# Optimization experiments

Measured on AMD Instinct MI355X. Metric: run time of the kernel, lower is better.

## Reference

```python
import jax, jax.numpy as jnp
import numpy as np

T, D_IN, H, E = 8192, 2048, 2048, 512


def setup_inputs() -> dict:
    key = jax.random.key(0)
    k_x, k_wi, k_wh, k_wo = jax.random.split(key, 4)
    s_in = 1.0 / np.sqrt(D_IN)
    s_h = 1.0 / np.sqrt(H)
    return {
        "inputs": jax.random.normal(k_x, (T, D_IN), dtype=jnp.float32),
        "w_i": jax.random.normal(k_wi, (D_IN, 3 * H), dtype=jnp.float32) * s_in,
        "w_h": jax.random.normal(k_wh, (H, 3 * H), dtype=jnp.float32) * s_h,
        "b": jnp.zeros((3 * H,), dtype=jnp.float32),
        "w_out": jax.random.normal(k_wo, (H, E), dtype=jnp.float32) * s_h,
        "b_out": jnp.zeros((E,), dtype=jnp.float32),
    }


def reference(inputs, w_i, w_h, b, w_out, b_out):
    h_size = w_h.shape[0]
    w_h_zr = w_h[:, : 2 * h_size]   # [H, 2H]
    w_h_a = w_h[:, 2 * h_size :]    # [H, H]
    b_zr = b[: 2 * h_size]
    b_a = b[2 * h_size :]

    def step(h, x):
        gates_x = x @ w_i                       # [3H]
        zr_x = gates_x[: 2 * h_size]
        a_x = gates_x[2 * h_size :]
        zr = jax.nn.sigmoid(zr_x + h @ w_h_zr + b_zr)
        z, r = zr[:h_size], zr[h_size:]
        a = jnp.tanh(a_x + (r * h) @ w_h_a + b_a)
        h_new = (1.0 - z) * h + z * a
        return h_new, None

    h0 = jnp.zeros((h_size,), dtype=inputs.dtype)
    h_final, _ = jax.lax.scan(step, h0, inputs)
    return h_final @ w_out + b_out
```

## Files before the change

### kernel.cpp

```cpp
#include <hip/hip_runtime.h>
#include <stdint.h>

#define T_STEPS 8192
#define DIN     2048
#define HD      2048
#define G3      6144
#define EOUT    512

#define NA 64
#define NB 64
#define HP 1024
#define NREP 8
#define SPIN_MAX (1<<20)

typedef unsigned long long u64;
typedef __attribute__((ext_vector_type(8))) __bf16 bf16x8;
typedef __attribute__((ext_vector_type(8))) unsigned short u16x8;
typedef __attribute__((ext_vector_type(4))) float f32x4;

__device__ __forceinline__ uint16_t f2bf(float v){
  uint32_t x = __float_as_uint(v);
  return (uint16_t)((x + 0x7fffu + ((x >> 16) & 1u)) >> 16);
}

__device__ __forceinline__ u64 aload(const u64* p){
  return __hip_atomic_load(p, __ATOMIC_RELAXED, __HIP_MEMORY_SCOPE_AGENT);
}
__device__ __forceinline__ void astore(u64* p, u64 v){
  __hip_atomic_store(p, v, __ATOMIC_RELAXED, __HIP_MEMORY_SCOPE_AGENT);
}

__device__ __forceinline__ void poll2(const u64* p0, const u64* p1, uint32_t want,
                                      u64& r0, u64& r1, volatile int* deadp){
  u64 a0 = aload(p0), a1 = aload(p1);
  int spins = 0;
  for(;;){
    u64 b0 = aload(p0), b1 = aload(p1);
    if ((uint32_t)(a0 >> 32) >= want && (uint32_t)(a1 >> 32) >= want) break;
    if ((++spins & 63) == 0){
      if (*deadp) break;
      if (spins > SPIN_MAX){ *deadp = 1; break; }
    }
    a0 = b0; a1 = b1;
  }
  r0 = a0; r1 = a1;
}

__device__ __forceinline__ bf16x8 load_afrag(const float* __restrict__ w, int col, int kb){
  u16x8 r;
  #pragma unroll
  for (int j = 0; j < 8; ++j)
    r[j] = f2bf(w[(size_t)(kb + j)*G3 + col]);
  return __builtin_bit_cast(bf16x8, r);
}

__device__ __forceinline__ void mv_pass(const uint32_t* vp_base,
                                        const bf16x8* wA, const bf16x8* wB,
                                        float* red, int wid, int lane){
  const uint32_t* vp = vp_base + wid*128;
  const int boff = (lane >> 4) << 2;
  f32x4 acc0 = {0.f,0.f,0.f,0.f}, acc1 = {0.f,0.f,0.f,0.f};
  #pragma unroll
  for (int s = 0; s < 8; ++s){
    uint4 bu = *(const uint4*)(vp + s*16 + boff);
    bf16x8 bf = __builtin_bit_cast(bf16x8, bu);
    acc0 = __builtin_amdgcn_mfma_f32_16x16x32_bf16(wA[s], bf, acc0, 0, 0, 0);
    acc1 = __builtin_amdgcn_mfma_f32_16x16x32_bf16(wB[s], bf, acc1, 0, 0, 0);
  }
  if ((lane & 15) == 0){
    int mb = (lane >> 4) << 2;
    #pragma unroll
    for (int r = 0; r < 4; ++r){
      red[(mb + r)*9 + wid]      = acc0[r];
      red[(16 + mb + r)*9 + wid] = acc1[r];
    }
  }
}

__global__ __launch_bounds__(512) void gates_gemm(const float* __restrict__ A,
                                                  const float* __restrict__ B,
                                                  float* __restrict__ C){
  __shared__ uint16_t Asb[128*40];
  __shared__ uint16_t Bsb[128*40];
  const int bm = blockIdx.x / (G3/128);
  const int bn = blockIdx.x % (G3/128);
  const int row0 = bm*128, col0 = bn*128;
  const int tid  = threadIdx.x;
  const int lane = tid & 63, wid = tid >> 6;
  const int wr = wid >> 2, wc = wid & 3;
  f32x4 acc[4][2] = {};
  for (int k0 = 0; k0 < DIN; k0 += 32){
    {
      int m = tid >> 2, ks = (tid & 3) * 8;
      const float* src = A + (size_t)(row0 + m)*DIN + k0 + ks;
      float4 f0 = *(const float4*)src;
      float4 f1 = *(const float4*)(src + 4);
      u16x8 pk;
      pk[0]=f2bf(f0.x); pk[1]=f2bf(f0.y); pk[2]=f2bf(f0.z); pk[3]=f2bf(f0.w);
      pk[4]=f2bf(f1.x); pk[5]=f2bf(f1.y); pk[6]=f2bf(f1.z); pk[7]=f2bf(f1.w);
      *(u16x8*)(Asb + m*40 + ks) = pk;
    }
    {
      int k = tid >> 4, n8 = tid & 15;
      const float* src = B + (size_t)(k0 + k)*G3 + col0 + n8;
      #pragma unroll
      for (int i = 0; i < 8; ++i)
        Bsb[(n8 + 16*i)*40 + k] = f2bf(src[16*i]);
    }
    __syncthreads();
    const int mrow = wr*64, ncol = wc*32;
    const int fm = lane & 15, fk = (lane >> 4) * 8;
    bf16x8 bfr[2];
    #pragma unroll
    for (int j = 0; j < 2; ++j)
      bfr[j] = *(const bf16x8*)(Bsb + (ncol + j*16 + fm)*40 + fk);
    #pragma unroll
    for (int i = 0; i < 4; ++i){
      bf16x8 af = *(const bf16x8*)(Asb + (mrow + i*16 + fm)*40 + fk);
      acc[i][0] = __builtin_amdgcn_mfma_f32_16x16x32_bf16(af, bfr[0], acc[i][0], 0,0,0);
      acc[i][1] = __builtin_amdgcn_mfma_f32_16x16x32_bf16(af, bfr[1], acc[i][1], 0,0,0);
    }
    __syncthreads();
  }
  const int mrow = row0 + wr*64, ncol = col0 + wc*32;
  #pragma unroll
  for (int i = 0; i < 4; ++i)
    #pragma unroll
    for (int j = 0; j < 2; ++j){
      int cc = ncol + j*16 + (lane & 15);
      int rr = mrow + i*16 + (lane >> 4)*4;
      #pragma unroll
      for (int q = 0; q < 4; ++q)
        C[(size_t)(rr + q)*G3 + cc] = acc[i][j][q];
    }
}

__global__ __launch_bounds__(512) void scan_kernel(
    const float* __restrict__ gates, const float* __restrict__ w_h,
    const float* __restrict__ b,
    u64* hbuf, u64* rhbuf, float* hfinal)
{
  __shared__ uint32_t vph[2][1024];
  __shared__ uint32_t vprh[2][1024];
  __shared__ float    red0[32*9];
  __shared__ float    red1[32*9];
  __shared__ float    gx[2][64];
  __shared__ float    hloc[2][32];
  __shared__ int      dead;
  volatile int* deadp = &dead;

  const int tid  = threadIdx.x;
  const int lane = tid & 63;
  const int wid  = tid >> 6;
  const bool isA = blockIdx.x < NA;
  const int  g   = isA ? (int)blockIdx.x : (int)blockIdx.x - NA;
  const int  rep = blockIdx.x & (NREP - 1);

  bf16x8 w0[8], w1[8], w2[8], w3[8];
  {
    const int kb0 = wid*256 + ((lane >> 4) << 3);
    const int c0  = isA ? (2048 + 32*g) : (32*g);
    #pragma unroll
    for (int s = 0; s < 8; ++s){
      w0[s] = load_afrag(w_h, c0 + (lane & 15),      kb0 + s*32);
      w1[s] = load_afrag(w_h, c0 + 16 + (lane & 15), kb0 + s*32);
    }
    if (!isA){
      const int ca = 4096 + 32*g;
      #pragma unroll
      for (int s = 0; s < 8; ++s){
        w2[s] = load_afrag(w_h, ca + (lane & 15),      kb0 + s*32);
        w3[s] = load_afrag(w_h, ca + 16 + (lane & 15), kb0 + s*32);
      }
    }
  }

  if (tid == 0) *deadp = 0;
  if (tid < 64) ((float*)hloc)[tid] = 0.f;

  int   gcol = -1;
  float bias = 0.f;
  if (isA) { if (tid < 32) gcol = 2048 + 32*g + tid; }
  else     { if (tid < 32)      gcol = 32*g + tid;
             else if (tid < 64) gcol = 4096 + 32*g + (tid - 32);}
  if (gcol >= 0) { bias = b[gcol]; gx[0][tid] = gates[gcol] + bias; }
  __syncthreads();

  for (int t = 0; t < T_STEPS; ++t){
    const int par = t & 1;

    {
      const u64* src = hbuf + ((size_t)(rep*2 + par))*HP;
      u64 v0, v1;
      poll2(src + tid, src + tid + 512, (uint32_t)t, v0, v1, deadp);
      vph[par][tid]       = (uint32_t)v0;
      vph[par][tid + 512] = (uint32_t)v1;
    }
    __syncthreads();
    if (*deadp) break;

    if (isA){
      mv_pass(&vph[par][0], w0, w1, red0, wid, lane);
      __syncthreads();
      if (tid < 32){
        float acc = 0.f;
        #pragma unroll
        for (int w = 0; w < 8; ++w) acc += red0[tid*9 + w];
        float pre = acc + gx[par][tid];
        float r = 1.f / (1.f + __expf(-pre));
        int col = 32*g + tid;
        uint32_t hp = vph[par][col >> 1];
        float hval = __uint_as_float((col & 1) ? (hp & 0xffff0000u) : (hp << 16));
        float rh = r * hval;
        float other = __shfl_xor(rh, 1);
        if (!(tid & 1)){
          u64 pv = ((u64)(uint32_t)(t + 1) << 32)
                 | ((u64)f2bf(other) << 16) | (u64)f2bf(rh);
          size_t idx = (size_t)(col >> 1);
          #pragma unroll
          for (int rp = 0; rp < NREP; ++rp)
            astore(rhbuf + (size_t)(rp*2 + par)*HP + idx, pv);
        }
        int tn = (t + 1 < T_STEPS) ? t + 1 : t;
        gx[par ^ 1][tid] = gates[(size_t)tn*G3 + gcol] + bias;
      }
    } else {
      mv_pass(&vph[par][0], w0, w1, red0, wid, lane);
      {
        const u64* src = rhbuf + ((size_t)(rep*2 + par))*HP;
        u64 v0, v1;
        poll2(src + tid, src + tid + 512, (uint32_t)(t + 1), v0, v1, deadp);
        vprh[par][tid]       = (uint32_t)v0;
        vprh[par][tid + 512] = (uint32_t)v1;
      }
      __syncthreads();
      if (*deadp) break;
      mv_pass(&vprh[par][0], w2, w3, red1, wid, lane);
      __syncthreads();
      if (tid < 32){
        float zacc = 0.f, aacc = 0.f;
        #pragma unroll
        for (int w = 0; w < 8; ++w){ zacc += red0[tid*9 + w]; aacc += red1[tid*9 + w]; }
        float z = 1.f / (1.f + __expf(-(zacc + gx[par][tid])));
        float apre = aacc + gx[par][32 + tid];
        float e = __expf(2.f*apre);
        float a = 1.f - 2.f/(1.f + e);
        float hold = hloc[par][tid];
        float hnew = hold + z*(a - hold);
        hloc[par ^ 1][tid] = hnew;
        float other = __shfl_xor(hnew, 1);
        if (!(tid & 1)){
          u64 pv = ((u64)(uint32_t)(t + 1) << 32)
                 | ((u64)f2bf(other) << 16) | (u64)f2bf(hnew);
          size_t idx = (size_t)((32*g + tid) >> 1);
          #pragma unroll
          for (int rp = 0; rp < NREP; ++rp)
            astore(hbuf + (size_t)(rp*2 + ((t+1)&1))*HP + idx, pv);
        }
      }
      if (gcol >= 0){
        int tn = (t + 1 < T_STEPS) ? t + 1 : t;
        gx[par ^ 1][tid] = gates[(size_t)tn*G3 + gcol] + bias;
      }
    }
  }

  if (!isA && tid < 32) hfinal[32*g + tid] = hloc[0][tid];
}

__global__ __launch_bounds__(1024) void out_proj(const float* __restrict__ hfin,
                                                 const float* __restrict__ w_out,
                                                 const float* __restrict__ b_out,
                                                 float* __restrict__ out){
  __shared__ float red[16][80];
  const int g  = blockIdx.x;
  const int cl = threadIdx.x & 63;
  const int kc = threadIdx.x >> 6;
  const int col = 64*g + cl;
  float acc = 0.f;
  for (int k = kc*128; k < kc*128 + 128; ++k)
    acc = fmaf(hfin[k], w_out[(size_t)k*EOUT + col], acc);
  red[kc][cl] = acc;
  __syncthreads();
  if (kc == 0){
    float s = 0.f;
    #pragma unroll
    for (int q = 0; q < 16; ++q) s += red[q][cl];
    out[col] = s + b_out[col];
  }
}

extern "C" void kernel_launch(void* const* d_in, const int* in_sizes, int n_in,
                              void* d_out, int out_size, void* d_ws, size_t ws_size,
                              hipStream_t stream) {
  const float* x     = (const float*)d_in[0];
  const float* w_i   = (const float*)d_in[1];
  const float* w_h   = (const float*)d_in[2];
  const float* b     = (const float*)d_in[3];
  const float* w_out = (const float*)d_in[4];
  const float* b_out = (const float*)d_in[5];
  float* out = (float*)d_out;

  float* gates  = (float*)d_ws;
  u64*   hbuf   = (u64*)(gates + (size_t)T_STEPS * G3);
  u64*   rhbuf  = hbuf + (size_t)NREP*2*HP;
  float* hfinal = (float*)(rhbuf + (size_t)NREP*2*HP);
  (void)in_sizes; (void)n_in; (void)out_size; (void)ws_size;

  hipMemsetAsync(hbuf, 0, (size_t)(2*NREP*2*HP)*sizeof(u64), stream);

  gates_gemm<<<dim3((T_STEPS/128)*(G3/128)), dim3(512), 0, stream>>>(x, w_i, gates);

  const float* gates_c = gates;
  void* kargs[6];
  kargs[0] = (void*)&gates_c;
  kargs[1] = (void*)&w_h;
  kargs[2] = (void*)&b;
  kargs[3] = (void*)&hbuf;
  kargs[4] = (void*)&rhbuf;
  kargs[5] = (void*)&hfinal;
  hipLaunchCooperativeKernel((void*)scan_kernel, dim3(NA + NB), dim3(512), kargs, 0u, stream);

  out_proj<<<dim3(EOUT/64), dim3(1024), 0, stream>>>(hfinal, w_out, b_out, out);
}
```

Measured before the change: 31.22 ms.

## Poll per-wave hidden-state slices to drop block barriers in GRU recurrence

Each wave now polls only the 128-entry slice of the hidden and r*h vectors it consumes in its MFMA pass, using a wave-wide __all check, instead of the whole block polling the full vector and meeting at a __syncthreads. This removes several block barriers per timestep and lets waves start their matvec as soon as their own slice arrives. Wave 0 in the A blocks also fetches its own h values directly so it no longer reads other waves' LDS. A short s_sleep in the spin loop reduces memory polling pressure but may add wake-up latency.

```diff
diff --git a/kernel.cpp b/kernel.cpp
--- a/kernel.cpp
+++ b/kernel.cpp
@@ -28,22 +28,6 @@
 }
 __device__ __forceinline__ void astore(u64* p, u64 v){
   __hip_atomic_store(p, v, __ATOMIC_RELAXED, __HIP_MEMORY_SCOPE_AGENT);
-}
-
-__device__ __forceinline__ void poll2(const u64* p0, const u64* p1, uint32_t want,
-                                      u64& r0, u64& r1, volatile int* deadp){
-  u64 a0 = aload(p0), a1 = aload(p1);
-  int spins = 0;
-  for(;;){
-    u64 b0 = aload(p0), b1 = aload(p1);
-    if ((uint32_t)(a0 >> 32) >= want && (uint32_t)(a1 >> 32) >= want) break;
-    if ((++spins & 63) == 0){
-      if (*deadp) break;
-      if (spins > SPIN_MAX){ *deadp = 1; break; }
-    }
-    a0 = b0; a1 = b1;
-  }
-  r0 = a0; r1 = a1;
 }
 
 __device__ __forceinline__ bf16x8 load_afrag(const float* __restrict__ w, int col, int kb){
@@ -54,10 +38,36 @@
   return __builtin_bit_cast(bf16x8, r);
 }
 
-__device__ __forceinline__ void mv_pass(const uint32_t* vp_base,
+template<bool OWN>
+__device__ __forceinline__ u64 poll_slice(const u64* src, uint32_t want,
+                                          uint32_t* lds_slice, int own_base,
+                                          int lane, volatile int* deadp){
+  const u64* p0 = src + 2*lane;
+  const u64* p1 = p0 + 1;
+  const u64* po = src + own_base + lane;
+  const bool need_own = OWN && (lane < 16);
+  u64 v0, v1, vo = 0;
+  int spins = 0;
+  for(;;){
+    v0 = aload(p0); v1 = aload(p1);
+    if (need_own) vo = aload(po);
+    bool ok = (uint32_t)(v0 >> 32) >= want && (uint32_t)(v1 >> 32) >= want &&
+              (!need_own || (uint32_t)(vo >> 32) >= want);
+    if (__all(ok)) break;
+    if ((++spins & 63) == 0){
+      if (*deadp) break;
+      if (spins > SPIN_MAX){ *deadp = 1; break; }
+    }
+    __builtin_amdgcn_s_sleep(1);
+  }
+  u64 pk = ((u64)(uint32_t)v1 << 32) | (u64)(uint32_t)v0;
+  *(u64*)&lds_slice[2*lane] = pk;
+  return vo;
+}
+
+__device__ __forceinline__ void mv_pass(const uint32_t* vp,
                                         const bf16x8* wA, const bf16x8* wB,
                                         float* red, int wid, int lane){
-  const uint32_t* vp = vp_base + wid*128;
   const int boff = (lane >> 4) << 2;
   f32x4 acc0 = {0.f,0.f,0.f,0.f}, acc1 = {0.f,0.f,0.f,0.f};
   #pragma unroll
@@ -189,78 +199,73 @@
   for (int t = 0; t < T_STEPS; ++t){
     const int par = t & 1;
 
-    {
+    if (isA){
       const u64* src = hbuf + ((size_t)(rep*2 + par))*HP;
-      u64 v0, v1;
-      poll2(src + tid, src + tid + 512, (uint32_t)t, v0, v1, deadp);
-      vph[par][tid]       = (uint32_t)v0;
-      vph[par][tid + 512] = (uint32_t)v1;
-    }
-    __syncthreads();
-    if (*deadp) break;
-
-    if (isA){
-      mv_pass(&vph[par][0], w0, w1, red0, wid, lane);
+      u64 vo;
+      if (wid == 0)
+        vo = poll_slice<true >(src, (uint32_t)t, &vph[par][0],       16*g, lane, deadp);
+      else
+        vo = poll_slice<false>(src + wid*128, (uint32_t)t,
+                               &vph[par][wid*128], 0, lane, deadp);
+      mv_pass(&vph[par][wid*128], w0, w1, red0, wid, lane);
       __syncthreads();
-      if (tid < 32){
-        float acc = 0.f;
-        #pragma unroll
-        for (int w = 0; w < 8; ++w) acc += red0[tid*9 + w];
-        float pre = acc + gx[par][tid];
-        float r = 1.f / (1.f + __expf(-pre));
-        int col = 32*g + tid;
-        uint32_t hp = vph[par][col >> 1];
-        float hval = __uint_as_float((col & 1) ? (hp & 0xffff0000u) : (hp << 16));
-        float rh = r * hval;
-        float other = __shfl_xor(rh, 1);
-        if (!(tid & 1)){
-          u64 pv = ((u64)(uint32_t)(t + 1) << 32)
-                 | ((u64)f2bf(other) << 16) | (u64)f2bf(rh);
-          size_t idx = (size_t)(col >> 1);
+      if (*deadp) break;
+      if (wid == 0){
+        uint32_t hp = __shfl((int)(uint32_t)vo, lane >> 1);
+        if (lane < 32){
+          float acc = 0.f;
           #pragma unroll
-          for (int rp = 0; rp < NREP; ++rp)
-            astore(rhbuf + (size_t)(rp*2 + par)*HP + idx, pv);
+          for (int w = 0; w < 8; ++w) acc += red0[lane*9 + w];
+          float pre = acc + gx[par][lane];
+          float r = 1.f / (1.f + __expf(-pre));
+          float hval = __uint_as_float((lane & 1) ? (hp & 0xffff0000u) : (hp << 16));
+          float rh = r * hval;
+          float other = __shfl_xor(rh, 1);
+          if (!(lane & 1)){
+            u64 pv = ((u64)(uint32_t)(t + 1) << 32)
+                   | ((u64)f2bf(other) << 16) | (u64)f2bf(rh);
+            size_t idx = (size_t)((32*g + lane) >> 1);
+            #pragma unroll
+            for (int rp = 0; rp < NREP; ++rp)
+              astore(rhbuf + (size_t)(rp*2 + par)*HP + idx, pv);
+          }
+          int tn = (t + 1 < T_STEPS) ? t + 1 : t;
+          gx[par ^ 1][lane] = gates[(size_t)tn*G3 + gcol] + bias;
         }
-        int tn = (t + 1 < T_STEPS) ? t + 1 : t;
-        gx[par ^ 1][tid] = gates[(size_t)tn*G3 + gcol] + bias;
       }
     } else {
-      mv_pass(&vph[par][0], w0, w1, red0, wid, lane);
-      {
-        const u64* src = rhbuf + ((size_t)(rep*2 + par))*HP;
-        u64 v0, v1;
-        poll2(src + tid, src + tid + 512, (uint32_t)(t + 1), v0, v1, deadp);
-        vprh[par][tid]       = (uint32_t)v0;
-        vprh[par][tid + 512] = (uint32_t)v1;
-      }
+      const u64* hsrc = hbuf + ((size_t)(rep*2 + par))*HP;
+      poll_slice<false>(hsrc + wid*128, (uint32_t)t, &vph[par][wid*128], 0, lane, deadp);
+      mv_pass(&vph[par][wid*128], w0, w1, red0, wid, lane);
+      const u64* rsrc = rhbuf + ((size_t)(rep*2 + par))*HP;
+      poll_slice<false>(rsrc + wid*128, (uint32_t)(t + 1), &vprh[par][wid*128], 0, lane, deadp);
+      mv_pass(&vprh[par][wid*128], w2, w3, red1, wid, lane);
       __syncthreads();
       if (*deadp) break;
-      mv_pass(&vprh[par][0], w2, w3, red1, wid, lane);
-      __syncthreads();
-      if (tid < 32){
+      if (wid == 0 && lane < 32){
         float zacc = 0.f, aacc = 0.f;
         #pragma unroll
-        for (int w = 0; w < 8; ++w){ zacc += red0[tid*9 + w]; aacc += red1[tid*9 + w]; }
-        float z = 1.f / (1.f + __expf(-(zacc + gx[par][tid])));
-        float apre = aacc + gx[par][32 + tid];
+        for (int w = 0; w < 8; ++w){ zacc += red0[lane*9 + w]; aacc += red1[lane*9 + w]; }
+        float z = 1.f / (1.f + __expf(-(zacc + gx[par][lane])));
+        float apre = aacc + gx[par][32 + lane];
         float e = __expf(2.f*apre);
         float a = 1.f - 2.f/(1.f + e);
-        float hold = hloc[par][tid];
+        float hold = hloc[par][lane];
         float hnew = hold + z*(a - hold);
-        hloc[par ^ 1][tid] = hnew;
+        hloc[par ^ 1][lane] = hnew;
         float other = __shfl_xor(hnew, 1);
-        if (!(tid & 1)){
+        if (!(lane & 1)){
           u64 pv = ((u64)(uint32_t)(t + 1) << 32)
                  | ((u64)f2bf(other) << 16) | (u64)f2bf(hnew);
-          size_t idx = (size_t)((32*g + tid) >> 1);
+          size_t idx = (size_t)((32*g + lane) >> 1);
           #pragma unroll
           for (int rp = 0; rp < NREP; ++rp)
             astore(hbuf + (size_t)(rp*2 + ((t+1)&1))*HP + idx, pv);
         }
       }
-      if (gcol >= 0){
+      if (wid == 0 && gcol >= 0){
         int tn = (t + 1 < T_STEPS) ? t + 1 : t;
-        gx[par ^ 1][tid] = gates[(size_t)tn*G3 + gcol] + bias;
+        gx[par ^ 1][lane] = gates[(size_t)tn*G3 + gcol] + bias;
       }
     }
   }
```

Result: faster. 27.59 ms, median of 5 (-11.6%).
